# Kernel tuning notes

Hardware: AMD Instinct MI355X
Metric: run time of the kernel (lower is better)

The kernel has to match this reference:

```python
import jax, jax.numpy as jnp
import numpy as np

DIST_THRESH = 0.1
W_DIST = 0.05
W_CHAMFER = 0.05
W_SEP = 0.0005


def setup_inputs() -> dict:
    key = jax.random.key(0)
    k1, k2, k3, k4 = jax.random.split(key, 4)
    B, N, K = 4, 200000, 64
    return {
        "landmarks_C": jax.random.uniform(k1, (B, N, 3), jnp.float32),          # predicted point coords
        "landmarks_F": jax.random.normal(k2, (B, N, 4), jnp.float32) * 0.05,    # [dist, dx, dy, dz]
        "targets_C": jax.random.uniform(k3, (B, K, 3), jnp.float32),            # GT landmark coords
        "targets_F": jax.random.randint(k4, (B, K), 0, 8),                      # GT landmark class labels
        "classes": jnp.arange(6),                                               # classes to supervise
    }


def reference(landmarks_C, landmarks_F, targets_C, targets_F, classes):
    def per_batch(C_i, F_i, tC, tF):
        # class mask over GT landmarks (replaces boolean indexing in torch)
        mask_k = jnp.any(tF[None, :] == classes[:, None], axis=0)          # [K]
        n_valid = mask_k.sum()
        dists_i = F_i[:, 0]                                                # predicted distance, [N]
        coords_i = C_i + F_i[:, 1:]                                        # refined coords, [N,3]
        # pairwise dists GT landmarks -> raw point coords, invalid classes pushed to +inf
        pd = jnp.linalg.norm(C_i[None, :, :] - tC[:, None, :], axis=-1)    # [K,N]
        pd = jnp.where(mask_k[:, None], pd, jnp.inf)
        min_d = pd.min(axis=0)                                             # [N]
        pm = min_d < DIST_THRESH                                           # points near some GT landmark
        # smooth-L1 (beta=1, sum) on predicted distance; clip(inf)=2*thresh reproduces empty-target fallback
        tgt = jnp.clip(min_d, 0.0, 2.0 * DIST_THRESH)
        diff = dists_i - tgt
        ad = jnp.abs(diff)
        dist_loss = jnp.where(ad < 1.0, 0.5 * diff * diff, ad - 0.5).sum()
        # pairwise dists GT landmarks -> refined coords
        ld = jnp.linalg.norm(coords_i[None, :, :] - tC[:, None, :], axis=-1)  # [K,N]
        ld_m = jnp.where(mask_k[:, None], ld, jnp.inf)
        p2g = jnp.where(pm, ld_m.min(axis=0), 0.0)                         # pred->gt, masked points only
        g2p = jnp.where(mask_k, ld_m.min(axis=1), 0.0)                     # gt->pred, valid GT only
        chamfer = (p2g * p2g).sum() + (g2p * g2p).sum()
        # separation: ratio of dists to 2 nearest (valid) GT landmarks, per masked point
        _, idx = jax.lax.top_k(-pd.T, 2)                                   # [N,2] indices of 2 smallest
        d01 = jnp.take_along_axis(ld.T, idx, axis=1)                       # [N,2]
        sep = jnp.where(pm, d01[:, 0] / d01[:, 1], 0.0).sum()
        sep = jnp.where(n_valid >= 2, sep, 0.0)
        return W_DIST * dist_loss + W_CHAMFER * chamfer + W_SEP * sep

    losses = jax.vmap(per_batch)(landmarks_C, landmarks_F, targets_C, targets_F)
    return losses.mean()
```

## Files before the change

### kernel.cpp

```cpp
#include <hip/hip_runtime.h>


constexpr int KT = 64;
constexpr int P  = 4;
constexpr int NREP = 16;
constexpr float DIST_THRESH = 0.1f;
constexpr float W_DIST    = 0.05f;
constexpr float W_CHAMFER = 0.05f;
constexpr float W_SEP     = 0.0005f;
constexpr float PT_SENT = -1e18f;
constexpr float TG_SENT = -1e18f;
constexpr float BIGF  = 3.0e38f;
constexpr float WBIAS = 16.0f;

typedef float f2 __attribute__((ext_vector_type(2)));

__device__ __forceinline__ unsigned umin_(unsigned a, unsigned b) { return a < b ? a : b; }
__device__ __forceinline__ unsigned umax_(unsigned a, unsigned b) { return a > b ? a : b; }

__device__ __forceinline__ f2 pk_fma(f2 a, f2 b, f2 c) {
#if __has_builtin(__builtin_elementwise_fma)
    return __builtin_elementwise_fma(a, b, c);
#else
    f2 r; r.x = fmaf(a.x, b.x, c.x); r.y = fmaf(a.y, b.y, c.y); return r;
#endif
}

__global__ __launch_bounds__(128, 6)
void landmark_main(const float* __restrict__ C, const float* __restrict__ F,
                   const float* __restrict__ tC, const int* __restrict__ tF,
                   const int* __restrict__ classes, int n_classes,
                   int N, unsigned int* __restrict__ g2p_rep,
                   float* __restrict__ sums_rep)
{
    __shared__ float4 tgtH[2][32];
    __shared__ float4 tgtFull[KT];
    __shared__ unsigned g2pLDS[KT];
    __shared__ uint4  mK1[64];
    __shared__ uint4  mK2[64];
    __shared__ float4 mLM[64];

    const int tid   = threadIdx.x;
    const int lane  = tid & 63;
    const int h     = tid >> 6;
    const int l31   = lane & 31;
    const int blk   = blockIdx.x;
    const int b     = blk & 3;
    const int chunk = blk >> 2;
    const int rep   = chunk & (NREP - 1);
    const unsigned kbase = (unsigned)(h << 5);

    if (tid < KT) {
        int f = tF[b * KT + tid];
        bool valid = false;
        for (int c = 0; c < n_classes; ++c) valid = valid || (f == classes[c]);
        float x = TG_SENT, y = TG_SENT, z = TG_SENT;
        if (valid) {
            x = tC[(b * KT + tid) * 3 + 0];
            y = tC[(b * KT + tid) * 3 + 1];
            z = tC[(b * KT + tid) * 3 + 2];
        }
        float4 v = make_float4(-2.f * x, -2.f * y, -2.f * z,
                               x * x + y * y + z * z + WBIAS);
        tgtFull[tid] = v;
        tgtH[tid >> 5][tid & 31] = v;
        g2pLDS[tid] = 0x7F7FFFFFu;
    }
    __syncthreads();

    const float*  Cb = C + (size_t)b * N * 3;
    const float4* Fb = (const float4*)(F + (size_t)b * N * 4);
    const int base = chunk * (64 * P);

    f2 pcx[P], pcy[P], pcz[P];
    float ppm[P], ccm[P], f0[P];
    bool  vp[P];
    #pragma unroll
    for (int p = 0; p < P; ++p) {
        int n = base + p * 64 + lane;
        bool v = (n < N);
        vp[p] = v;
        int ni = v ? n : 0;
        float4 f4 = Fb[ni];
        float X = Cb[3 * ni + 0], Y = Cb[3 * ni + 1], Z = Cb[3 * ni + 2];
        f0[p] = f4.x;
        if (!v) { X = PT_SENT; Y = PT_SENT; Z = PT_SENT; f4.y = f4.z = f4.w = 0.f; }
        float cxv = X + f4.y, cyv = Y + f4.z, czv = Z + f4.w;
        pcx[p] = (f2){X, cxv};
        pcy[p] = (f2){Y, cyv};
        pcz[p] = (f2){Z, czv};
        ppm[p] = fmaf(Z, Z, fmaf(Y, Y, X * X)) - WBIAS;
        ccm[p] = fmaf(czv, czv, fmaf(cyv, cyv, cxv * cxv)) - WBIAS;
    }

    unsigned k1[P], k2[P];
    float lmin[P];
    #pragma unroll
    for (int p = 0; p < P; ++p) { k1[p] = 0xFFFFFFFFu; k2[p] = 0xFFFFFFFFu; lmin[p] = BIGF; }

    #pragma unroll 8
    for (int i = 0; i < 32; ++i) {
        const unsigned kk = (unsigned)(l31 ^ i);
        const float4 T = tgtH[h][kk];
        const unsigned tk = kk | kbase;
        const f2 Tx = {T.x, T.x}, Ty = {T.y, T.y}, Tz = {T.z, T.z}, Tw = {T.w, T.w};
        float a0, a1, a2, a3;
        #pragma unroll
        for (int p = 0; p < P; ++p) {
            f2 w = pk_fma(pcx[p], Tx, pk_fma(pcy[p], Ty, pk_fma(pcz[p], Tz, Tw)));
            unsigned key = (__float_as_uint(w.x) & 0xFFFFFFC0u) | tk;
            unsigned hi = umax_(k1[p], key);
            k1[p] = umin_(k1[p], key);
            k2[p] = umin_(k2[p], hi);
            lmin[p] = fminf(lmin[p], w.y);
            float av = w.y + ccm[p];
            if (p == 0) a0 = av; else if (p == 1) a1 = av;
            else if (p == 2) a2 = av; else a3 = av;
        }
        float dl = fmaxf(fminf(fminf(a0, a1), fminf(a2, a3)), 0.f);
        atomicMin(&g2pLDS[tk], __float_as_uint(dl));
    }

    if (h == 0) {
        mK1[lane] = make_uint4(k1[0], k1[1], k1[2], k1[3]);
        mK2[lane] = make_uint4(k2[0], k2[1], k2[2], k2[3]);
        mLM[lane] = make_float4(lmin[0], lmin[1], lmin[2], lmin[3]);
    }
    __syncthreads();

    if (h == 0) {
        atomicMax(&g2p_rep[rep * 256 + b * 64 + lane], ~g2pLDS[lane]);
    } else {
        uint4 A1 = mK1[lane], A2 = mK2[lane];
        float4 AL = mLM[lane];
        const unsigned a1v[P] = {A1.x, A1.y, A1.z, A1.w};
        const unsigned a2v[P] = {A2.x, A2.y, A2.z, A2.w};
        const float    alv[P] = {AL.x, AL.y, AL.z, AL.w};

        float dist_acc = 0.f, p2g_acc = 0.f, sep_acc = 0.f;
        #pragma unroll
        for (int p = 0; p < P; ++p) {
            unsigned m1 = umin_(a1v[p], k1[p]);
            unsigned m2 = umin_(umax_(a1v[p], k1[p]), umin_(a2v[p], k2[p]));
            float lm = fminf(alv[p], lmin[p]);
            float keyf1 = __uint_as_float(m1 & 0xFFFFFFC0u);
            float mind = sqrtf(fmaxf(keyf1 + ppm[p], 0.f));
            bool pm = (mind < DIST_THRESH) && vp[p];
            float tgtv = fminf(mind, 2.0f * DIST_THRESH);
            float diff = f0[p] - tgtv;
            float ad = fabsf(diff);
            float sl1 = (ad < 1.0f) ? 0.5f * diff * diff : (ad - 0.5f);
            if (vp[p]) dist_acc += sl1;
            if (pm) {
                p2g_acc += fmaxf(lm + ccm[p], 0.f);
                int i1 = (int)(m1 & 63u), i2 = (int)(m2 & 63u);
                float4 T1 = tgtFull[i1], T2 = tgtFull[i2];
                float cxv = pcx[p].y, cyv = pcy[p].y, czv = pcz[p].y;
                float l1sq = fmaf(cxv, T1.x, fmaf(cyv, T1.y, fmaf(czv, T1.z, T1.w))) + ccm[p];
                float l2sq = fmaf(cxv, T2.x, fmaf(cyv, T2.y, fmaf(czv, T2.z, T2.w))) + ccm[p];
                sep_acc += sqrtf(fmaxf(l1sq, 0.f) / fmaxf(l2sq, 1e-30f));
            }
        }

        float v0 = dist_acc, v1 = p2g_acc, v2 = sep_acc;
        #pragma unroll
        for (int o = 32; o > 0; o >>= 1) {
            v0 += __shfl_down(v0, o, 64);
            v1 += __shfl_down(v1, o, 64);
            v2 += __shfl_down(v2, o, 64);
        }
        if (lane == 0) {
            float* sb = sums_rep + rep * 16 + b;
            atomicAdd(sb + 0, v0);
            atomicAdd(sb + 4, v1);
            atomicAdd(sb + 8, v2);
        }
    }
}

__global__ void landmark_finalize(const int* __restrict__ tF, const int* __restrict__ classes,
                                  int n_classes, const unsigned int* __restrict__ g2p_rep,
                                  const float* __restrict__ sums_rep, float* __restrict__ out)
{
    __shared__ float lossb[4];
    const int tid = threadIdx.x;
    const int b = tid >> 6, k = tid & 63;

    int f = tF[b * KT + k];
    bool valid = false;
    for (int c = 0; c < n_classes; ++c) valid = valid || (f == classes[c]);

    unsigned enc = 0;
    for (int r = 0; r < NREP; ++r) enc = umax_(enc, g2p_rep[r * 256 + b * 64 + k]);
    float g  = valid ? __uint_as_float(~enc) : 0.f;
    float nv = valid ? 1.f : 0.f;

    #pragma unroll
    for (int o = 32; o > 0; o >>= 1) {
        g  += __shfl_down(g, o, 64);
        nv += __shfl_down(nv, o, 64);
    }
    if (k == 0) {
        float sd = 0.f, sp = 0.f, ss = 0.f;
        for (int r = 0; r < NREP; ++r) {
            sd += sums_rep[r * 16 + 0 + b];
            sp += sums_rep[r * 16 + 4 + b];
            ss += sums_rep[r * 16 + 8 + b];
        }
        float sep = (nv >= 2.f) ? ss : 0.f;
        lossb[b] = W_DIST * sd + W_CHAMFER * (sp + g) + W_SEP * sep;
    }
    __syncthreads();
    if (tid == 0)
        out[0] = (lossb[0] + lossb[1] + lossb[2] + lossb[3]) * 0.25f;
}

extern "C" void kernel_launch(void* const* d_in, const int* in_sizes, int n_in,
                              void* d_out, int out_size, void* d_ws, size_t ws_size,
                              hipStream_t stream)
{
    const float* C       = (const float*)d_in[0];
    const float* F       = (const float*)d_in[1];
    const float* tC      = (const float*)d_in[2];
    const int*   tF      = (const int*)d_in[3];
    const int*   classes = (const int*)d_in[4];
    const int n_classes = in_sizes[4];
    const int B = 4;
    const int N = in_sizes[0] / (3 * B);

    unsigned int* g2p_rep  = (unsigned int*)d_ws;
    float*        sums_rep = (float*)((char*)d_ws + NREP * 256 * 4);

    hipMemsetAsync(d_ws, 0, NREP * 256 * 4 + NREP * 16 * 4, stream);

    const int cpb = (N + 64 * P - 1) / (64 * P);
    landmark_main<<<cpb * 4, 128, 0, stream>>>(C, F, tC, tF, classes, n_classes,
                                               N, g2p_rep, sums_rep);
    landmark_finalize<<<1, 256, 0, stream>>>(tF, classes, n_classes, g2p_rep,
                                             sums_rep, (float*)d_out);
}
```

Measured before the change: 99.29 us.

## Double points per thread and replace XOR target indexing with duplicated LDS rotation

Each thread now handles 8 points instead of 4, so every target load from shared memory is reused across twice as many points and there are half as many blocks and per-target atomics. The XOR-swizzled target index becomes a rotation into a duplicated 64-entry copy of each half's targets. Per-point validity flags and squared norms are dropped from registers: invalid points get a sentinel f0 so they add no loss, and the squared norm is recomputed in the epilogue. The cost is higher register pressure, with the occupancy hint lowered from 6 to 3 blocks, and fewer blocks in flight.

```diff
diff --git a/kernel.cpp b/kernel.cpp
--- a/kernel.cpp
+++ b/kernel.cpp
@@ -2,7 +2,7 @@
 
 
 constexpr int KT = 64;
-constexpr int P  = 4;
+constexpr int P  = 8;
 constexpr int NREP = 16;
 constexpr float DIST_THRESH = 0.1f;
 constexpr float W_DIST    = 0.05f;
@@ -26,19 +26,19 @@
 #endif
 }
 
-__global__ __launch_bounds__(128, 6)
+__global__ __launch_bounds__(128, 3)
 void landmark_main(const float* __restrict__ C, const float* __restrict__ F,
                    const float* __restrict__ tC, const int* __restrict__ tF,
                    const int* __restrict__ classes, int n_classes,
                    int N, unsigned int* __restrict__ g2p_rep,
                    float* __restrict__ sums_rep)
 {
-    __shared__ float4 tgtH[2][32];
+    __shared__ float4 tgtH2[2][64];
     __shared__ float4 tgtFull[KT];
     __shared__ unsigned g2pLDS[KT];
-    __shared__ uint4  mK1[64];
-    __shared__ uint4  mK2[64];
-    __shared__ float4 mLM[64];
+    __shared__ unsigned mK1[64][P];
+    __shared__ unsigned mK2[64][P];
+    __shared__ float    mLM[64][P];
 
     const int tid   = threadIdx.x;
     const int lane  = tid & 63;
@@ -63,7 +63,9 @@
         float4 v = make_float4(-2.f * x, -2.f * y, -2.f * z,
                                x * x + y * y + z * z + WBIAS);
         tgtFull[tid] = v;
-        tgtH[tid >> 5][tid & 31] = v;
+        int hh = tid >> 5, j = tid & 31;
+        tgtH2[hh][j] = v;
+        tgtH2[hh][j + 32] = v;
         g2pLDS[tid] = 0x7F7FFFFFu;
     }
     __syncthreads();
@@ -73,23 +75,20 @@
     const int base = chunk * (64 * P);
 
     f2 pcx[P], pcy[P], pcz[P];
-    float ppm[P], ccm[P], f0[P];
-    bool  vp[P];
+    float ccm[P], f0[P];
     #pragma unroll
     for (int p = 0; p < P; ++p) {
         int n = base + p * 64 + lane;
         bool v = (n < N);
-        vp[p] = v;
         int ni = v ? n : 0;
         float4 f4 = Fb[ni];
         float X = Cb[3 * ni + 0], Y = Cb[3 * ni + 1], Z = Cb[3 * ni + 2];
-        f0[p] = f4.x;
+        f0[p] = v ? f4.x : 2.0f * DIST_THRESH;
         if (!v) { X = PT_SENT; Y = PT_SENT; Z = PT_SENT; f4.y = f4.z = f4.w = 0.f; }
         float cxv = X + f4.y, cyv = Y + f4.z, czv = Z + f4.w;
         pcx[p] = (f2){X, cxv};
         pcy[p] = (f2){Y, cyv};
         pcz[p] = (f2){Z, czv};
-        ppm[p] = fmaf(Z, Z, fmaf(Y, Y, X * X)) - WBIAS;
         ccm[p] = fmaf(czv, czv, fmaf(cyv, cyv, cxv * cxv)) - WBIAS;
     }
 
@@ -98,13 +97,14 @@
     #pragma unroll
     for (int p = 0; p < P; ++p) { k1[p] = 0xFFFFFFFFu; k2[p] = 0xFFFFFFFFu; lmin[p] = BIGF; }
 
-    #pragma unroll 8
+    const float4* TH = tgtH2[h];
+
+    #pragma unroll 4
     for (int i = 0; i < 32; ++i) {
-        const unsigned kk = (unsigned)(l31 ^ i);
-        const float4 T = tgtH[h][kk];
-        const unsigned tk = kk | kbase;
+        const float4 T = TH[l31 + i];
+        const unsigned tk = kbase | (unsigned)((l31 + i) & 31);
         const f2 Tx = {T.x, T.x}, Ty = {T.y, T.y}, Tz = {T.z, T.z}, Tw = {T.w, T.w};
-        float a0, a1, a2, a3;
+        float av[P];
         #pragma unroll
         for (int p = 0; p < P; ++p) {
             f2 w = pk_fma(pcx[p], Tx, pk_fma(pcy[p], Ty, pk_fma(pcz[p], Tz, Tw)));
@@ -113,44 +113,44 @@
             k1[p] = umin_(k1[p], key);
             k2[p] = umin_(k2[p], hi);
             lmin[p] = fminf(lmin[p], w.y);
-            float av = w.y + ccm[p];
-            if (p == 0) a0 = av; else if (p == 1) a1 = av;
-            else if (p == 2) a2 = av; else a3 = av;
-        }
-        float dl = fmaxf(fminf(fminf(a0, a1), fminf(a2, a3)), 0.f);
+            av[p] = w.y + ccm[p];
+        }
+        float dl = fminf(fminf(fminf(av[0], av[1]), fminf(av[2], av[3])),
+                         fminf(fminf(av[4], av[5]), fminf(av[6], av[7])));
+        dl = fmaxf(dl, 0.f);
         atomicMin(&g2pLDS[tk], __float_as_uint(dl));
     }
 
     if (h == 0) {
-        mK1[lane] = make_uint4(k1[0], k1[1], k1[2], k1[3]);
-        mK2[lane] = make_uint4(k2[0], k2[1], k2[2], k2[3]);
-        mLM[lane] = make_float4(lmin[0], lmin[1], lmin[2], lmin[3]);
+        #pragma unroll
+        for (int p = 0; p < P; ++p) {
+            mK1[lane][p] = k1[p];
+            mK2[lane][p] = k2[p];
+            mLM[lane][p] = lmin[p];
+        }
     }
     __syncthreads();
 
     if (h == 0) {
         atomicMax(&g2p_rep[rep * 256 + b * 64 + lane], ~g2pLDS[lane]);
     } else {
-        uint4 A1 = mK1[lane], A2 = mK2[lane];
-        float4 AL = mLM[lane];
-        const unsigned a1v[P] = {A1.x, A1.y, A1.z, A1.w};
-        const unsigned a2v[P] = {A2.x, A2.y, A2.z, A2.w};
-        const float    alv[P] = {AL.x, AL.y, AL.z, AL.w};
-
         float dist_acc = 0.f, p2g_acc = 0.f, sep_acc = 0.f;
         #pragma unroll
         for (int p = 0; p < P; ++p) {
-            unsigned m1 = umin_(a1v[p], k1[p]);
-            unsigned m2 = umin_(umax_(a1v[p], k1[p]), umin_(a2v[p], k2[p]));
-            float lm = fminf(alv[p], lmin[p]);
+            unsigned a1 = mK1[lane][p], a2 = mK2[lane][p];
+            float    al = mLM[lane][p];
+            unsigned m1 = umin_(a1, k1[p]);
+            unsigned m2 = umin_(umax_(a1, k1[p]), umin_(a2, k2[p]));
+            float lm = fminf(al, lmin[p]);
+            float X = pcx[p].x, Y = pcy[p].x, Z = pcz[p].x;
+            float ppm = fmaf(Z, Z, fmaf(Y, Y, X * X)) - WBIAS;
             float keyf1 = __uint_as_float(m1 & 0xFFFFFFC0u);
-            float mind = sqrtf(fmaxf(keyf1 + ppm[p], 0.f));
-            bool pm = (mind < DIST_THRESH) && vp[p];
+            float mind = sqrtf(fmaxf(keyf1 + ppm, 0.f));
+            bool pm = mind < DIST_THRESH;
             float tgtv = fminf(mind, 2.0f * DIST_THRESH);
             float diff = f0[p] - tgtv;
             float ad = fabsf(diff);
-            float sl1 = (ad < 1.0f) ? 0.5f * diff * diff : (ad - 0.5f);
-            if (vp[p]) dist_acc += sl1;
+            dist_acc += (ad < 1.0f) ? 0.5f * diff * diff : (ad - 0.5f);
             if (pm) {
                 p2g_acc += fmaxf(lm + ccm[p], 0.f);
                 int i1 = (int)(m1 & 63u), i2 = (int)(m2 & 63u);
```

After: 103.7 us. +4.4%, slower.
